# Kernel optimization log

Measured on AMD Instinct MI355X. Metric: run time of the kernel, lower is better.

Reference implementation:

```python
import jax, jax.numpy as jnp
import numpy as np

HID = 64   # RNN_HID_SIZE
FEAT = 9   # feature dim, hard-coded in module
T = 36     # SEQ_LEN


def setup_inputs() -> dict:
    key = jax.random.key(0)
    ks = jax.random.split(key, 20)
    B = 16384

    def u(k, shape, stdv):
        return jax.random.uniform(k, shape, jnp.float32, -stdv, stdv)

    s_h = 1.0 / np.sqrt(HID)    # stdv for layers with 64 rows / fan-in 64
    s_f = 1.0 / np.sqrt(FEAT)   # stdv 1/3 for feature-sized layers
    s_c = 1.0 / np.sqrt(2 * FEAT)  # weight_combine: Linear(18, 9)

    inp = {
        "values": jax.random.normal(ks[0], (B, T, FEAT), jnp.float32),
        "masks": (jax.random.uniform(ks[1], (B, T, FEAT)) < 0.8).astype(jnp.float32),
        "deltas": jax.random.uniform(ks[2], (B, T, FEAT), jnp.float32, 0.0, 5.0),
        # TemporalDecay h: W [64, 9], stdv = 1/sqrt(64)
        "W_gh": u(ks[3], (HID, FEAT), s_h), "b_gh": u(ks[4], (HID,), s_h),
        # TemporalDecay x (diag): W [9, 9], stdv = 1/sqrt(9)
        "W_gx": u(ks[5], (FEAT, FEAT), s_f), "b_gx": u(ks[6], (FEAT,), s_f),
        # hist_reg: Linear(64, 9)
        "W_hist": u(ks[7], (FEAT, HID), s_h), "b_hist": u(ks[8], (FEAT,), s_h),
        "W_feat": u(ks[9], (FEAT, FEAT), s_f), "b_feat": u(ks[10], (FEAT,), s_f),
        # weight_combine: Linear(18, 9)
        "W_comb": u(ks[11], (FEAT, 2 * FEAT), s_c), "b_comb": u(ks[12], (FEAT,), s_c),
        # LSTMCell(18, 64): gates order i, f, g, o
        "W_ih": u(ks[13], (4 * HID, 2 * FEAT), s_h), "W_hh": u(ks[14], (4 * HID, HID), s_h),
        "b_ih": u(ks[15], (4 * HID,), s_h), "b_hh": u(ks[16], (4 * HID,), s_h),
    }
    return inp


def reference(values, masks, deltas, W_gh, b_gh, W_gx, b_gx, W_hist, b_hist,
              W_feat, b_feat, W_comb, b_comb, W_ih, W_hh, b_ih, b_hh):
    B = values.shape[0]
    dt = values.dtype
    eye = jnp.eye(FEAT, dtype=dt)
    Wgx_diag = W_gx * eye            # TemporalDecay diag mask
    Wfeat_off = W_feat * (1.0 - eye)

    # time-major for scan: [T, B, F]
    xs = (jnp.swapaxes(values, 0, 1), jnp.swapaxes(masks, 0, 1), jnp.swapaxes(deltas, 0, 1))

    def step(carry, xt):
        h, c, loss = carry
        x, m, d = xt
        gamma_h = jnp.exp(-jax.nn.relu(d @ W_gh.T + b_gh))   # [B, 64]
        gamma_x = jnp.exp(-jax.nn.relu(d @ Wgx_diag.T + b_gx))  # [B, 9]
        h = h * gamma_h
        x_h = h @ W_hist.T + b_hist
        denom = jnp.sum(m) + 1e-5
        x_c = m * x + (1.0 - m) * x_h
        z_h = x_c @ Wfeat_off.T + b_feat
        alpha = jnp.concatenate([gamma_x, m], axis=1) @ W_comb.T + b_comb
        c_h = alpha * z_h + (1.0 - alpha) * x_h
        loss = loss + (jnp.sum(jnp.abs(x - x_h) * m)
                       + jnp.sum(jnp.abs(x - z_h) * m)
                       + jnp.sum(jnp.abs(x - c_h) * m)) / denom
        c_c = m * x + (1.0 - m) * c_h
        inp = jnp.concatenate([c_c, m], axis=1)              # [B, 18]
        gates = inp @ W_ih.T + b_ih + h @ W_hh.T + b_hh      # [B, 256]
        i, f, g, o = jnp.split(gates, 4, axis=1)
        c = jax.nn.sigmoid(f) * c + jax.nn.sigmoid(i) * jnp.tanh(g)
        h = jax.nn.sigmoid(o) * jnp.tanh(c)
        return (h, c, loss), c_c

    init = (jnp.zeros((B, HID), dt), jnp.zeros((B, HID), dt), jnp.zeros((), dt))
    (_, _, loss), imps = jax.lax.scan(step, init, xs)
    imputations = jnp.swapaxes(imps, 0, 1)  # [B, T, F]
    return loss / T, imputations
```

## Files before the change

### kernel.cpp

```cpp
#include <hip/hip_runtime.h>

typedef _Float16 hh;
typedef _Float16 h2  __attribute__((ext_vector_type(2)));
typedef _Float16 v4h __attribute__((ext_vector_type(4)));
typedef _Float16 v8h __attribute__((ext_vector_type(8)));
typedef float v4f    __attribute__((ext_vector_type(4)));
typedef unsigned short u16;

#define T_STEPS 36
#define FEAT 9
#define HID 64
#define BT 32
#define SIN_STR 232
#define PK_STR 40

__device__ __forceinline__ float fast_exp2(float x) {
#if __has_builtin(__builtin_amdgcn_exp2f)
  return __builtin_amdgcn_exp2f(x);
#else
  return exp2f(x);
#endif
}
__device__ __forceinline__ float fast_rcp(float x) {
#if __has_builtin(__builtin_amdgcn_rcpf)
  return __builtin_amdgcn_rcpf(x);
#else
  return 1.f / x;
#endif
}
__device__ __forceinline__ float sigmoid_fast(float x) {
  return fast_rcp(1.f + fast_exp2(x * -1.442695041f));
}
__device__ __forceinline__ float tanh_fast(float x) {
  return 1.f - 2.f * fast_rcp(1.f + fast_exp2(x * 2.885390082f));
}
__device__ __forceinline__ float fdot2(h2 a, h2 b, float c) {
#if __has_builtin(__builtin_amdgcn_fdot2)
  return __builtin_amdgcn_fdot2(a, b, c, false);
#else
  return c + (float)a[0] * (float)b[0] + (float)a[1] * (float)b[1];
#endif
}
__device__ __forceinline__ h2 mkh2(hh a, hh b) { h2 r; r[0] = a; r[1] = b; return r; }
__device__ __forceinline__ v4f mfma16(v8h a, v8h b, v4f c) {
  return __builtin_amdgcn_mfma_f32_16x16x32_f16(a, b, c, 0, 0, 0);
}

__global__ void zero_ws(float* __restrict__ ws, float* __restrict__ out) {
  int tid = threadIdx.x;
  if (tid < T_STEPS) ws[tid] = 0.f;
  if (tid == 0) out[0] = 0.f;
}

__global__ __launch_bounds__(256) void denom_kernel(const float* __restrict__ masks,
                                                    float* __restrict__ ws) {
  __shared__ float red[T_STEPS];
  const int tid = threadIdx.x;
  if (tid < T_STEPS) red[tid] = 0.f;
  __syncthreads();
  const int idx = blockIdx.x * 256 + tid;
  const int t0 = (idx % 9) * 4;
  const float4* p = (const float4*)masks + (size_t)idx * 9;
  float acc[4] = {0.f, 0.f, 0.f, 0.f};
#pragma unroll
  for (int c = 0; c < 9; ++c) {
    float4 v = p[c];
    acc[(4 * c) / 9]     += v.x;
    acc[(4 * c + 1) / 9] += v.y;
    acc[(4 * c + 2) / 9] += v.z;
    acc[(4 * c + 3) / 9] += v.w;
  }
#pragma unroll
  for (int j = 0; j < 4; ++j) atomicAdd(&red[t0 + j], acc[j]);
  __syncthreads();
  if (tid < T_STEPS) atomicAdd(&ws[tid], red[tid]);
}

#define BARX() asm volatile("s_waitcnt lgkmcnt(0)\n\ts_barrier" ::: "memory")

#define RITS_STEP(t, pxC,pmC,pdC,pxCb,pmCb,pdCb, pxN,pmN,pdN,pxNb,pmNb,pdNb)   \
  {                                                                            \
    const float inv_den = fast_rcp(denom[(t)] + 1e-5f);                        \
        \
    v4f gacc[2];                                                               \
    {                                                                          \
      const int sel = ((t) + 1) & 1;                                           \
      const int awin = 176 + sel * 24;                                         \
      _Pragma("unroll")                                                        \
      for (int mt = 0; mt < 2; ++mt) {                                         \
        v8h a_ = *(const v8h*)&sIn[(mt * 16 + nlo) * SIN_STR + awin + q * 8];  \
        v4f z4 = {0.f, 0.f, 0.f, 0.f};                                         \
        gacc[mt] = sel ? mfma16(a_, bGamB, z4) : mfma16(a_, bGamA, z4);        \
      }                                                                        \
    }                                                                          \
    if (wid < 2) {                                                             \
      const int base_ = ((t) & 1) * 96;                                        \
      v4f xacc = {0.f, 0.f, 0.f, 0.f};                                         \
      _Pragma("unroll")                                                        \
      for (int kt = 0; kt < 3; ++kt) {                                         \
        v8h a_ = *(const v8h*)&sIn[(wid * 16 + nlo) * SIN_STR + base_ +        \
                                   kt * 32 + q * 8];                           \
        xacc = mfma16(a_, bH[kt], xacc);                                       \
      }                                                                        \
      if (nlo < 9) {                                                           \
        _Pragma("unroll")                                                      \
        for (int r = 0; r < 4; ++r)                                            \
          sPk[(wid * 16 + q * 4 + r) * PK_STR + 18 + nlo] = (hh)xacc[r];       \
      }                                                                        \
    }                                                                          \
    BARX();                                                                    \
        \
    {                                                                          \
      const int pk = eP * PK_STR;                                              \
      float x_f  = (float)sPk[pk + fqw];                                       \
      float m_f  = (float)sPk[pk + 9 + fqw];                                   \
      float xh_f = (float)sPk[pk + 18 + fqw];                                  \
      v8h r0 = *(const v8h*)&sPk[pk];                                          \
      v8h r1 = *(const v8h*)&sPk[pk + 8];                                      \
      v8h r2 = *(const v8h*)&sPk[pk + 16];                                     \
      v8h r3 = *(const v8h*)&sPk[pk + 24];                                     \
      v4h r4 = *(const v4h*)&sPk[pk + 32];                                     \
      hh xxh[9] = {r0[0],r0[1],r0[2],r0[3],r0[4],r0[5],r0[6],r0[7],r1[0]};     \
      hh mmh[9] = {r1[1],r1[2],r1[3],r1[4],r1[5],r1[6],r1[7],r2[0],r2[1]};     \
      hh xhh[9] = {r2[2],r2[3],r2[4],r2[5],r2[6],r2[7],r3[0],r3[1],r3[2]};     \
      hh ddh[9] = {r3[3],r3[4],r3[5],r3[6],r3[7],r4[0],r4[1],r4[2],r4[3]};     \
      hh xch[10];                                                              \
      _Pragma("unroll")                                                        \
      for (int f = 0; f < 9; ++f) {                                            \
        u16 mb = __builtin_bit_cast(u16, mmh[f]);                              \
        xch[f] = mb ? xxh[f] : xhh[f];                                         \
      }                                                                        \
      xch[9] = (hh)0.f;                                                        \
      hh gxh[9];                                                               \
      _Pragma("unroll")                                                        \
      for (int f = 0; f < 9; ++f) {                                            \
        float y = fmaxf((float)ddh[f] * wgx[f] + bgxv[f], 0.f);                \
        gxh[f] = (hh)fast_exp2(y * -1.442695041f);                             \
      }                                                                        \
      h2 xc2[5] = {mkh2(xch[0],xch[1]), mkh2(xch[2],xch[3]),                   \
                   mkh2(xch[4],xch[5]), mkh2(xch[6],xch[7]),                   \
                   mkh2(xch[8],xch[9])};                                       \
      h2 g2[9]  = {mkh2(gxh[0],gxh[1]), mkh2(gxh[2],gxh[3]),                   \
                   mkh2(gxh[4],gxh[5]), mkh2(gxh[6],gxh[7]),                   \
                   mkh2(gxh[8],mmh[0]), mkh2(mmh[1],mmh[2]),                   \
                   mkh2(mmh[3],mmh[4]), mkh2(mmh[5],mmh[6]),                   \
                   mkh2(mmh[7],mmh[8])};                                       \
      float z1 = bf1, a1 = bc1v;                                               \
      _Pragma("unroll")                                                        \
      for (int j = 0; j < 5; ++j) z1 = fdot2(wf1[j], xc2[j], z1);              \
      _Pragma("unroll")                                                        \
      for (int j = 0; j < 9; ++j) a1 = fdot2(wc1[j], g2[j], a1);               \
      float ch1 = xh_f + a1 * (z1 - xh_f);                                     \
      bool obs1 = (m_f != 0.f);                                                \
      float cc1 = obs1 ? x_f : ch1;                                            \
      float lterm = obs1 ? (fabsf(x_f - xh_f) + fabsf(x_f - z1) +              \
                            fabsf(x_f - ch1)) : 0.f;                           \
      const int pb = ((t) & 1) * 96;                                           \
      sIn[eP * SIN_STR + pb + fqw] = (hh)cc1;                                  \
      sIn[eP * SIN_STR + pb + 9 + fqw] = (hh)m_f;                              \
      out[1 + (size_t)(b0 + eP) * (T_STEPS * FEAT) + (t) * FEAT + fqw] = cc1;  \
      if (fqw == 7) {                                                          \
        float z2 = bf2, a2 = bc2v;                                             \
        _Pragma("unroll")                                                      \
        for (int j = 0; j < 5; ++j) z2 = fdot2(wf2[j], xc2[j], z2);            \
        _Pragma("unroll")                                                      \
        for (int j = 0; j < 9; ++j) a2 = fdot2(wc2[j], g2[j], a2);             \
        float x8 = (float)xxh[8], m8 = (float)mmh[8], xh8 = (float)xhh[8];     \
        float ch2 = xh8 + a2 * (z2 - xh8);                                     \
        bool obs2 = (m8 != 0.f);                                               \
        float cc2 = obs2 ? x8 : ch2;                                           \
        lterm += obs2 ? (fabsf(x8 - xh8) + fabsf(x8 - z2) +                    \
                         fabsf(x8 - ch2)) : 0.f;                               \
        sIn[eP * SIN_STR + pb + 8] = (hh)cc2;                                  \
        sIn[eP * SIN_STR + pb + 17] = mmh[8];                                  \
        out[1 + (size_t)(b0 + eP) * (T_STEPS * FEAT) + (t) * FEAT + 8] = cc2;  \
      }                                                                        \
      loss_acc += lterm * inv_den;                                             \
    }                                                                          \
    BARX();                                                                    \
      \
    {                                                                          \
      const bool ldN = ((t) + 2 < T_STEPS);                                    \
      const bool ldD = ((t) + 3 < T_STEPS);                                    \
      if (ldN) {                                                               \
        size_t offn = (size_t)(b0 + e1) * (T_STEPS * FEAT) +                   \
                      ((t) + 2) * FEAT + f1;                                   \
        pxN = values[offn]; pmN = masks[offn];                                 \
        if (tid < 32) {                                                        \
          size_t offn2 = (size_t)(b0 + e2g) * (T_STEPS * FEAT) +               \
                         ((t) + 2) * FEAT + f2g;                               \
          pxNb = values[offn2]; pmNb = masks[offn2];                           \
        }                                                                      \
      }                                                                        \
      if (ldD) {                                                               \
        size_t offd = (size_t)(b0 + e1) * (T_STEPS * FEAT) +                   \
                      ((t) + 3) * FEAT + f1;                                   \
        pdN = deltas[offd];                                                    \
        if (tid < 32) {                                                        \
          size_t offd2 = (size_t)(b0 + e2g) * (T_STEPS * FEAT) +               \
                         ((t) + 3) * FEAT + f2g;                               \
          pdNb = deltas[offd2];                                                \
        }                                                                      \
      }                                                                        \
      const int base_ = ((t) & 1) * 96;                                        \
      const int pub = (((t) + 1) & 1) * 96;                                    \
      v8h af[2][3];                                                            \
      _Pragma("unroll")                                                        \
      for (int mt = 0; mt < 2; ++mt)                                           \
        _Pragma("unroll")                                                      \
        for (int kt = 0; kt < 3; ++kt)                                         \
          af[mt][kt] = *(const v8h*)&sIn[(mt * 16 + nlo) * SIN_STR + base_ +   \
                                         kt * 32 + q * 8];                     \
      v4f acc[2][4];                                                           \
      _Pragma("unroll")                                                        \
      for (int mt = 0; mt < 2; ++mt)                                           \
        _Pragma("unroll")                                                      \
        for (int p = 0; p < 4; ++p)                                            \
          acc[mt][p] = (v4f){0.f, 0.f, 0.f, 0.f};                              \
      _Pragma("unroll")                                                        \
      for (int mt = 0; mt < 2; ++mt)                                           \
        _Pragma("unroll")                                                      \
        for (int p = 0; p < 4; ++p)                                            \
          _Pragma("unroll")                                                    \
          for (int kt = 0; kt < 3; ++kt)                                       \
            acc[mt][p] = mfma16(af[mt][kt], bG[p][kt], acc[mt][p]);            \
      _Pragma("unroll")                                                        \
      for (int mt = 0; mt < 2; ++mt) {                                         \
        _Pragma("unroll")                                                      \
        for (int r = 0; r < 4; ++r) {                                          \
          float ig = sigmoid_fast(acc[mt][0][r]);                              \
          float fg = sigmoid_fast(acc[mt][1][r]);                              \
          float gg = tanh_fast(acc[mt][2][r]);                                 \
          float og = sigmoid_fast(acc[mt][3][r]);                              \
          float cn = fg * c_s[mt * 4 + r] + ig * gg;                           \
          c_s[mt * 4 + r] = cn;                                                \
          float hn = og * tanh_fast(cn);                                       \
          float gam = fast_exp2(fmaxf(gacc[mt][r], 0.f) * -1.442695041f);      \
          sIn[(mt * 16 + q * 4 + r) * SIN_STR + pub + 18 + j_col] =            \
              (hh)(hn * gam);                                                  \
        }                                                                      \
      }                                                                        \
      if ((t) + 1 < T_STEPS) {                                                 \
        sPk[e1 * PK_STR + f1] = (hh)pxC;                                       \
        sPk[e1 * PK_STR + 9 + f1] = (hh)pmC;                                   \
        sPk[e1 * PK_STR + 27 + f1] = (hh)dH;                                   \
        if (tid < 32) {                                                        \
          sPk[e2g * PK_STR + f2g] = (hh)pxCb;                                  \
          sPk[e2g * PK_STR + 9 + f2g] = (hh)pmCb;                              \
          sPk[e2g * PK_STR + 27 + f2g] = (hh)dHb;                              \
        }                                                                      \
      }                                                                        \
      if ((t) + 2 < T_STEPS) {                                                 \
        const int sb = 192 + ((t) & 1) * 10;                                   \
        sIn[e1 * SIN_STR + sb + f1] = (hh)pdC;                                 \
        if (tid < 32) sIn[e2g * SIN_STR + sb + f2g] = (hh)pdCb;                \
      }                                                                        \
      dH = pdC; dHb = pdCb;                                                    \
    }                                                                          \
    BARX();                                                                    \
  }

__global__ __launch_bounds__(256, 2) void rits_kernel(
    const float* __restrict__ values, const float* __restrict__ masks,
    const float* __restrict__ deltas,
    const float* __restrict__ W_gh, const float* __restrict__ b_gh,
    const float* __restrict__ W_gx, const float* __restrict__ b_gx,
    const float* __restrict__ W_hist, const float* __restrict__ b_hist,
    const float* __restrict__ W_feat, const float* __restrict__ b_feat,
    const float* __restrict__ W_comb, const float* __restrict__ b_comb,
    const float* __restrict__ W_ih, const float* __restrict__ W_hh,
    const float* __restrict__ b_ih, const float* __restrict__ b_hh,
    const float* __restrict__ denom, float* __restrict__ out) {

  __shared__ __align__(16) hh sIn[BT * SIN_STR];
  __shared__ __align__(16) hh sPk[BT * PK_STR];
  __shared__ float sRed[256];

  const int tid = threadIdx.x;
  const int lane = tid & 63;
  const int wid = tid >> 6;
  const int q = lane >> 4;
  const int nlo = lane & 15;
  const int b0 = blockIdx.x * BT;
  const int j_col = 16 * wid + nlo;

  v8h bG[4][3];
#pragma unroll
  for (int p = 0; p < 4; ++p)
#pragma unroll
    for (int kt = 0; kt < 3; ++kt) {
      int n = 64 * p + j_col;
      v8h r;
#pragma unroll
      for (int jj = 0; jj < 8; ++jj) {
        int k = kt * 32 + q * 8 + jj;
        float v = 0.f;
        if (k < 18)       v = W_ih[n * 18 + k];
        else if (k < 82)  v = W_hh[n * 64 + (k - 18)];
        else if (k == 82) v = b_ih[n] + b_hh[n];
        r[jj] = (hh)v;
      }
      bG[p][kt] = r;
    }
  v8h bH[3];
#pragma unroll
  for (int kt = 0; kt < 3; ++kt) {
    v8h r;
#pragma unroll
    for (int jj = 0; jj < 8; ++jj) {
      int k = kt * 32 + q * 8 + jj;
      float v = 0.f;
      if (nlo < 9) {
        if (k >= 18 && k < 82) v = W_hist[nlo * 64 + (k - 18)];
        else if (k == 82)      v = b_hist[nlo];
      }
      r[jj] = (hh)v;
    }
    bH[kt] = r;
  }
  v8h bGamA, bGamB;
  {
    int n = j_col;
    v8h ra, rb;
#pragma unroll
    for (int jj = 0; jj < 8; ++jj) {
      int k = q * 8 + jj;
      float va = 0.f, vb = 0.f;
      if (k == 2) va = b_gh[n];
      else if (k >= 16 && k < 25) va = W_gh[n * 9 + (k - 16)];
      if (k >= 2 && k < 11) vb = W_gh[n * 9 + (k - 2)];
      else if (k == 12) vb = b_gh[n];
      ra[jj] = (hh)va; rb[jj] = (hh)vb;
    }
    bGamA = ra; bGamB = rb;
  }

  const int eP = tid >> 3, fqw = tid & 7;
  h2 wf1[5], wf2[5], wc1[9], wc2[9];
  float bf1 = b_feat[fqw], bf2 = b_feat[8];
  float bc1v = b_comb[fqw], bc2v = b_comb[8];
#pragma unroll
  for (int j = 0; j < 5; ++j) {
    int i0 = 2 * j, i1 = 2 * j + 1;
    hh a0 = (hh)((i0 == fqw) ? 0.f : W_feat[fqw * 9 + i0]);
    hh a1 = (hh)((i1 < 9) ? ((i1 == fqw) ? 0.f : W_feat[fqw * 9 + i1]) : 0.f);
    wf1[j] = mkh2(a0, a1);
    hh c0 = (hh)((i0 == 8) ? 0.f : W_feat[8 * 9 + i0]);
    hh c1 = (hh)((i1 < 9) ? W_feat[8 * 9 + i1] : 0.f);
    wf2[j] = mkh2(c0, c1);
  }
#pragma unroll
  for (int j = 0; j < 9; ++j) {
    wc1[j] = mkh2((hh)W_comb[fqw * 18 + 2 * j], (hh)W_comb[fqw * 18 + 2 * j + 1]);
    wc2[j] = mkh2((hh)W_comb[8 * 18 + 2 * j], (hh)W_comb[8 * 18 + 2 * j + 1]);
  }
  float wgx[9], bgxv[9];
#pragma unroll
  for (int f = 0; f < 9; ++f) { wgx[f] = W_gx[f * 9 + f]; bgxv[f] = b_gx[f]; }

  for (int i = tid; i < BT * SIN_STR; i += 256) sIn[i] = (hh)0.f;
  __syncthreads();
  if (tid < BT) {
    sIn[tid * SIN_STR + 82] = (hh)1.f;
    sIn[tid * SIN_STR + 178] = (hh)1.f;
    sIn[tid * SIN_STR + 212] = (hh)1.f;
  }
  const int e1 = tid / 9, f1 = tid - 9 * e1;
  const int e2g = (tid + 256) / 9, f2g = (tid + 256) - 9 * e2g;
  float pA_x = 0.f, pA_m = 0.f, pA_d = 0.f, pA_xb = 0.f, pA_mb = 0.f, pA_db = 0.f;
  float pB_x = 0.f, pB_m = 0.f, pB_d = 0.f, pB_xb = 0.f, pB_mb = 0.f, pB_db = 0.f;
  float dH = 0.f, dHb = 0.f;
  {
    size_t off = (size_t)(b0 + e1) * (T_STEPS * FEAT) + f1;
    sPk[e1 * PK_STR + f1] = (hh)values[off];
    sPk[e1 * PK_STR + 9 + f1] = (hh)masks[off];
    sPk[e1 * PK_STR + 27 + f1] = (hh)deltas[off];
    float d1 = deltas[off + FEAT];
    dH = d1;
    sIn[e1 * SIN_STR + 202 + f1] = (hh)d1;
    pA_x = values[off + FEAT]; pA_m = masks[off + FEAT];
    pA_d = deltas[off + 2 * FEAT];
    if (tid < 32) {
      size_t off2 = (size_t)(b0 + e2g) * (T_STEPS * FEAT) + f2g;
      sPk[e2g * PK_STR + f2g] = (hh)values[off2];
      sPk[e2g * PK_STR + 9 + f2g] = (hh)masks[off2];
      sPk[e2g * PK_STR + 27 + f2g] = (hh)deltas[off2];
      float d1b = deltas[off2 + FEAT];
      dHb = d1b;
      sIn[e2g * SIN_STR + 202 + f2g] = (hh)d1b;
      pA_xb = values[off2 + FEAT]; pA_mb = masks[off2 + FEAT];
      pA_db = deltas[off2 + 2 * FEAT];
    }
  }
  __syncthreads();

  float c_s[8];
#pragma unroll
  for (int i = 0; i < 8; ++i) c_s[i] = 0.f;
  float loss_acc = 0.f;

  for (int t = 0; t < T_STEPS; t += 2) {
    RITS_STEP(t,     pA_x, pA_m, pA_d, pA_xb, pA_mb, pA_db,
                     pB_x, pB_m, pB_d, pB_xb, pB_mb, pB_db);
    RITS_STEP(t + 1, pB_x, pB_m, pB_d, pB_xb, pB_mb, pB_db,
                     pA_x, pA_m, pA_d, pA_xb, pA_mb, pA_db);
  }

  sRed[tid] = loss_acc;
  __syncthreads();
  for (int k = 128; k > 0; k >>= 1) {
    if (tid < k) sRed[tid] += sRed[tid + k];
    __syncthreads();
  }
  if (tid == 0) atomicAdd(out, sRed[0] * (1.f / (float)T_STEPS));
}

extern "C" void kernel_launch(void* const* d_in, const int* in_sizes, int n_in,
                              void* d_out, int out_size, void* d_ws, size_t ws_size,
                              hipStream_t stream) {
  const float* values = (const float*)d_in[0];
  const float* masks  = (const float*)d_in[1];
  const float* deltas = (const float*)d_in[2];
  const float* W_gh   = (const float*)d_in[3];
  const float* b_gh   = (const float*)d_in[4];
  const float* W_gx   = (const float*)d_in[5];
  const float* b_gx   = (const float*)d_in[6];
  const float* W_hist = (const float*)d_in[7];
  const float* b_hist = (const float*)d_in[8];
  const float* W_feat = (const float*)d_in[9];
  const float* b_feat = (const float*)d_in[10];
  const float* W_comb = (const float*)d_in[11];
  const float* b_comb = (const float*)d_in[12];
  const float* W_ih   = (const float*)d_in[13];
  const float* W_hh   = (const float*)d_in[14];
  const float* b_ih   = (const float*)d_in[15];
  const float* b_hh   = (const float*)d_in[16];

  float* out = (float*)d_out;
  float* ws  = (float*)d_ws;
  int B = in_sizes[0] / (T_STEPS * FEAT);

  zero_ws<<<1, 64, 0, stream>>>(ws, out);
  denom_kernel<<<(B * 9) / 256, 256, 0, stream>>>(masks, ws);
  rits_kernel<<<B / BT, 256, 0, stream>>>(values, masks, deltas,
                                          W_gh, b_gh, W_gx, b_gx,
                                          W_hist, b_hist, W_feat, b_feat,
                                          W_comb, b_comb, W_ih, W_hh,
                                          b_ih, b_hh, ws, out);
}
```

Measured before the change: 242.9 us.

## Drop per-step barrier by redundant x_h MFMA per wave; precompute gamma_x at staging

Every wave now computes the history-regression MFMA for its own row tile, so each wave has the x_h values it needs without the block barrier. That barrier is replaced by a local LDS wait. Gamma_x is now computed once per element when deltas are staged into shared memory, instead of redundantly (9 exps) per thread per step. The fdot2 chains are split into independent accumulators to shorten dependency latency. The trade-off is extra redundant MFMA work, and skipping the barrier may risk cross-wave data races on the shared buffers.

```diff
diff --git a/kernel.cpp b/kernel.cpp
--- a/kernel.cpp
+++ b/kernel.cpp
@@ -81,7 +81,8 @@
 #define RITS_STEP(t, pxC,pmC,pdC,pxCb,pmCb,pdCb, pxN,pmN,pdN,pxNb,pmNb,pdNb)   \
   {                                                                            \
     const float inv_den = fast_rcp(denom[(t)] + 1e-5f);                        \
-        \
+    const int pb = ((t) & 1) * 96;                                             \
+         \
     v4f gacc[2];                                                               \
     {                                                                          \
       const int sel = ((t) + 1) & 1;                                           \
@@ -93,23 +94,25 @@
         gacc[mt] = sel ? mfma16(a_, bGamB, z4) : mfma16(a_, bGamA, z4);        \
       }                                                                        \
     }                                                                          \
-    if (wid < 2) {                                                             \
-      const int base_ = ((t) & 1) * 96;                                        \
+       \
+    {                                                                          \
       v4f xacc = {0.f, 0.f, 0.f, 0.f};                                         \
       _Pragma("unroll")                                                        \
       for (int kt = 0; kt < 3; ++kt) {                                         \
-        v8h a_ = *(const v8h*)&sIn[(wid * 16 + nlo) * SIN_STR + base_ +        \
+        v8h a_ = *(const v8h*)&sIn[(mtw * 16 + nlo) * SIN_STR + pb +           \
                                    kt * 32 + q * 8];                           \
         xacc = mfma16(a_, bH[kt], xacc);                                       \
       }                                                                        \
-      if (nlo < 9) {                                                           \
+         \
+      if ((q >> 1) == (wid & 1) && nlo < 9) {                                  \
         _Pragma("unroll")                                                      \
         for (int r = 0; r < 4; ++r)                                            \
-          sPk[(wid * 16 + q * 4 + r) * PK_STR + 18 + nlo] = (hh)xacc[r];       \
+          sPk[(mtw * 16 + q * 4 + r) * PK_STR + 18 + nlo] = (hh)xacc[r];       \
       }                                                                        \
     }                                                                          \
-    BARX();                                                                    \
-        \
+           \
+    asm volatile("s_waitcnt lgkmcnt(0)" ::: "memory");                         \
+                 \
     {                                                                          \
       const int pk = eP * PK_STR;                                              \
       float x_f  = (float)sPk[pk + fqw];                                       \
@@ -123,7 +126,7 @@
       hh xxh[9] = {r0[0],r0[1],r0[2],r0[3],r0[4],r0[5],r0[6],r0[7],r1[0]};     \
       hh mmh[9] = {r1[1],r1[2],r1[3],r1[4],r1[5],r1[6],r1[7],r2[0],r2[1]};     \
       hh xhh[9] = {r2[2],r2[3],r2[4],r2[5],r2[6],r2[7],r3[0],r3[1],r3[2]};     \
-      hh ddh[9] = {r3[3],r3[4],r3[5],r3[6],r3[7],r4[0],r4[1],r4[2],r4[3]};     \
+      hh gxh[9] = {r3[3],r3[4],r3[5],r3[6],r3[7],r4[0],r4[1],r4[2],r4[3]};     \
       hh xch[10];                                                              \
       _Pragma("unroll")                                                        \
       for (int f = 0; f < 9; ++f) {                                            \
@@ -131,12 +134,6 @@
         xch[f] = mb ? xxh[f] : xhh[f];                                         \
       }                                                                        \
       xch[9] = (hh)0.f;                                                        \
-      hh gxh[9];                                                               \
-      _Pragma("unroll")                                                        \
-      for (int f = 0; f < 9; ++f) {                                            \
-        float y = fmaxf((float)ddh[f] * wgx[f] + bgxv[f], 0.f);                \
-        gxh[f] = (hh)fast_exp2(y * -1.442695041f);                             \
-      }                                                                        \
       h2 xc2[5] = {mkh2(xch[0],xch[1]), mkh2(xch[2],xch[3]),                   \
                    mkh2(xch[4],xch[5]), mkh2(xch[6],xch[7]),                   \
                    mkh2(xch[8],xch[9])};                                       \
@@ -145,26 +142,40 @@
                    mkh2(gxh[8],mmh[0]), mkh2(mmh[1],mmh[2]),                   \
                    mkh2(mmh[3],mmh[4]), mkh2(mmh[5],mmh[6]),                   \
                    mkh2(mmh[7],mmh[8])};                                       \
-      float z1 = bf1, a1 = bc1v;                                               \
-      _Pragma("unroll")                                                        \
-      for (int j = 0; j < 5; ++j) z1 = fdot2(wf1[j], xc2[j], z1);              \
-      _Pragma("unroll")                                                        \
-      for (int j = 0; j < 9; ++j) a1 = fdot2(wc1[j], g2[j], a1);               \
+                        \
+      float z1a = bf1, z1b = 0.f;                                              \
+      z1a = fdot2(wf1[0], xc2[0], z1a); z1b = fdot2(wf1[1], xc2[1], z1b);      \
+      z1a = fdot2(wf1[2], xc2[2], z1a); z1b = fdot2(wf1[3], xc2[3], z1b);      \
+      z1a = fdot2(wf1[4], xc2[4], z1a);                                        \
+      float z1 = z1a + z1b;                                                    \
+      float a1a = bc1v, a1b = 0.f, a1c = 0.f;                                  \
+      a1a = fdot2(wc1[0], g2[0], a1a); a1b = fdot2(wc1[1], g2[1], a1b);        \
+      a1c = fdot2(wc1[2], g2[2], a1c); a1a = fdot2(wc1[3], g2[3], a1a);        \
+      a1b = fdot2(wc1[4], g2[4], a1b); a1c = fdot2(wc1[5], g2[5], a1c);        \
+      a1a = fdot2(wc1[6], g2[6], a1a); a1b = fdot2(wc1[7], g2[7], a1b);        \
+      a1c = fdot2(wc1[8], g2[8], a1c);                                         \
+      float a1 = (a1a + a1b) + a1c;                                            \
       float ch1 = xh_f + a1 * (z1 - xh_f);                                     \
       bool obs1 = (m_f != 0.f);                                                \
       float cc1 = obs1 ? x_f : ch1;                                            \
       float lterm = obs1 ? (fabsf(x_f - xh_f) + fabsf(x_f - z1) +              \
                             fabsf(x_f - ch1)) : 0.f;                           \
-      const int pb = ((t) & 1) * 96;                                           \
       sIn[eP * SIN_STR + pb + fqw] = (hh)cc1;                                  \
       sIn[eP * SIN_STR + pb + 9 + fqw] = (hh)m_f;                              \
       out[1 + (size_t)(b0 + eP) * (T_STEPS * FEAT) + (t) * FEAT + fqw] = cc1;  \
       if (fqw == 7) {                                                          \
-        float z2 = bf2, a2 = bc2v;                                             \
-        _Pragma("unroll")                                                      \
-        for (int j = 0; j < 5; ++j) z2 = fdot2(wf2[j], xc2[j], z2);            \
-        _Pragma("unroll")                                                      \
-        for (int j = 0; j < 9; ++j) a2 = fdot2(wc2[j], g2[j], a2);             \
+        float z2a = bf2, z2b = 0.f;                                            \
+        z2a = fdot2(wf2[0], xc2[0], z2a); z2b = fdot2(wf2[1], xc2[1], z2b);    \
+        z2a = fdot2(wf2[2], xc2[2], z2a); z2b = fdot2(wf2[3], xc2[3], z2b);    \
+        z2a = fdot2(wf2[4], xc2[4], z2a);                                      \
+        float z2 = z2a + z2b;                                                  \
+        float a2a = bc2v, a2b = 0.f, a2c = 0.f;                                \
+        a2a = fdot2(wc2[0], g2[0], a2a); a2b = fdot2(wc2[1], g2[1], a2b);      \
+        a2c = fdot2(wc2[2], g2[2], a2c); a2a = fdot2(wc2[3], g2[3], a2a);      \
+        a2b = fdot2(wc2[4], g2[4], a2b); a2c = fdot2(wc2[5], g2[5], a2c);      \
+        a2a = fdot2(wc2[6], g2[6], a2a); a2b = fdot2(wc2[7], g2[7], a2b);      \
+        a2c = fdot2(wc2[8], g2[8], a2c);                                       \
+        float a2 = (a2a + a2b) + a2c;                                          \
         float x8 = (float)xxh[8], m8 = (float)mmh[8], xh8 = (float)xhh[8];     \
         float ch2 = xh8 + a2 * (z2 - xh8);                                     \
         bool obs2 = (m8 != 0.f);                                               \
@@ -202,14 +213,13 @@
           pdNb = deltas[offd2];                                                \
         }                                                                      \
       }                                                                        \
-      const int base_ = ((t) & 1) * 96;                                        \
       const int pub = (((t) + 1) & 1) * 96;                                    \
       v8h af[2][3];                                                            \
       _Pragma("unroll")                                                        \
       for (int mt = 0; mt < 2; ++mt)                                           \
         _Pragma("unroll")                                                      \
         for (int kt = 0; kt < 3; ++kt)                                         \
-          af[mt][kt] = *(const v8h*)&sIn[(mt * 16 + nlo) * SIN_STR + base_ +   \
+          af[mt][kt] = *(const v8h*)&sIn[(mt * 16 + nlo) * SIN_STR + pb +      \
                                          kt * 32 + q * 8];                     \
       v4f acc[2][4];                                                           \
       _Pragma("unroll")                                                        \
@@ -243,11 +253,13 @@
       if ((t) + 1 < T_STEPS) {                                                 \
         sPk[e1 * PK_STR + f1] = (hh)pxC;                                       \
         sPk[e1 * PK_STR + 9 + f1] = (hh)pmC;                                   \
-        sPk[e1 * PK_STR + 27 + f1] = (hh)dH;                                   \
+        sPk[e1 * PK_STR + 27 + f1] =                                           \
+            (hh)fast_exp2(fmaxf(dH * wgx1 + bgx1, 0.f) * -1.442695041f);       \
         if (tid < 32) {                                                        \
           sPk[e2g * PK_STR + f2g] = (hh)pxCb;                                  \
           sPk[e2g * PK_STR + 9 + f2g] = (hh)pmCb;                              \
-          sPk[e2g * PK_STR + 27 + f2g] = (hh)dHb;                              \
+          sPk[e2g * PK_STR + 27 + f2g] =                                       \
+              (hh)fast_exp2(fmaxf(dHb * wgx2 + bgx2, 0.f) * -1.442695041f);    \
         }                                                                      \
       }                                                                        \
       if ((t) + 2 < T_STEPS) {                                                 \
@@ -283,6 +295,7 @@
   const int nlo = lane & 15;
   const int b0 = blockIdx.x * BT;
   const int j_col = 16 * wid + nlo;
+  const int mtw = wid >> 1;
 
   v8h bG[4][3];
 #pragma unroll
@@ -354,9 +367,12 @@
     wc1[j] = mkh2((hh)W_comb[fqw * 18 + 2 * j], (hh)W_comb[fqw * 18 + 2 * j + 1]);
     wc2[j] = mkh2((hh)W_comb[8 * 18 + 2 * j], (hh)W_comb[8 * 18 + 2 * j + 1]);
   }
-  float wgx[9], bgxv[9];
-#pragma unroll
-  for (int f = 0; f < 9; ++f) { wgx[f] = W_gx[f * 9 + f]; bgxv[f] = b_gx[f]; }
+
+  const int e1 = tid / 9, f1 = tid - 9 * e1;
+  const int e2g = (tid + 256) / 9, f2g = (tid + 256) - 9 * e2g;
+  const float wgx1 = W_gx[f1 * 9 + f1], bgx1 = b_gx[f1];
+  float wgx2 = 0.f, bgx2 = 0.f;
+  if (tid < 32) { wgx2 = W_gx[f2g * 9 + f2g]; bgx2 = b_gx[f2g]; }
 
   for (int i = tid; i < BT * SIN_STR; i += 256) sIn[i] = (hh)0.f;
   __syncthreads();
@@ -365,16 +381,16 @@
     sIn[tid * SIN_STR + 178] = (hh)1.f;
     sIn[tid * SIN_STR + 212] = (hh)1.f;
   }
-  const int e1 = tid / 9, f1 = tid - 9 * e1;
-  const int e2g = (tid + 256) / 9, f2g = (tid + 256) - 9 * e2g;
   float pA_x = 0.f, pA_m = 0.f, pA_d = 0.f, pA_xb = 0.f, pA_mb = 0.f, pA_db = 0.f;
   float pB_x = 0.f, pB_m = 0.f, pB_d = 0.f, pB_xb = 0.f, pB_mb = 0.f, pB_db = 0.f;
   float dH = 0.f, dHb = 0.f;
   {
     size_t off = (size_t)(b0 + e1) * (T_STEPS * FEAT) + f1;
+    float d0 = deltas[off];
     sPk[e1 * PK_STR + f1] = (hh)values[off];
     sPk[e1 * PK_STR + 9 + f1] = (hh)masks[off];
-    sPk[e1 * PK_STR + 27 + f1] = (hh)deltas[off];
+    sPk[e1 * PK_STR + 27 + f1] =
+        (hh)fast_exp2(fmaxf(d0 * wgx1 + bgx1, 0.f) * -1.442695041f);
     float d1 = deltas[off + FEAT];
     dH = d1;
     sIn[e1 * SIN_STR + 202 + f1] = (hh)d1;
@@ -382,9 +398,11 @@
     pA_d = deltas[off + 2 * FEAT];
     if (tid < 32) {
       size_t off2 = (size_t)(b0 + e2g) * (T_STEPS * FEAT) + f2g;
+      float d0b = deltas[off2];
       sPk[e2g * PK_STR + f2g] = (hh)values[off2];
       sPk[e2g * PK_STR + 9 + f2g] = (hh)masks[off2];
-      sPk[e2g * PK_STR + 27 + f2g] = (hh)deltas[off2];
+      sPk[e2g * PK_STR + 27 + f2g] =
+          (hh)fast_exp2(fmaxf(d0b * wgx2 + bgx2, 0.f) * -1.442695041f);
       float d1b = deltas[off2 + FEAT];
       dHb = d1b;
       sIn[e2g * SIN_STR + 202 + f2g] = (hh)d1b;
```

New measurement: 245.4 us. Within noise of the previous version (+1.0%).

## Give each wavefront its own 16-row batch tile to drop block barriers

Applied to the files above, without the earlier changes.

The block work split changes from 4 waves sharing 32 batch rows (each wave owning a slice of hidden columns) to each wave owning an independent 16-row tile and computing all 256 gate columns. Workgroup s_barriers become wave-local LDS waitcnt fences, and the feature stage is split so each lane handles 3 features of one element. The gamma_x exponential is also precomputed when deltas are staged. In exchange, each wave holds 48 gate weight fragments and 16 cell-state values in registers, so launch bounds drop to one block per SIMD pair and occupancy falls.

```diff
diff --git a/kernel.cpp b/kernel.cpp
--- a/kernel.cpp
+++ b/kernel.cpp
@@ -10,7 +10,8 @@
 #define T_STEPS 36
 #define FEAT 9
 #define HID 64
-#define BT 32
+#define WT 16
+#define NW 4
 #define SIN_STR 232
 #define PK_STR 40
 
@@ -76,45 +77,44 @@
   if (tid < T_STEPS) atomicAdd(&ws[tid], red[tid]);
 }
 
-#define BARX() asm volatile("s_waitcnt lgkmcnt(0)\n\ts_barrier" ::: "memory")
-
-#define RITS_STEP(t, pxC,pmC,pdC,pxCb,pmCb,pdCb, pxN,pmN,pdN,pxNb,pmNb,pdNb)   \
+#define WFENCE() do { \
+  asm volatile("s_waitcnt lgkmcnt(0)" ::: "memory"); \
+  __builtin_amdgcn_sched_barrier(0); \
+} while (0)
+
+#define STEP(t, CUR, NXT)                                                      \
   {                                                                            \
     const float inv_den = fast_rcp(denom[(t)] + 1e-5f);                        \
-        \
-    v4f gacc[2];                                                               \
+    const int pb = ((t) & 1) * 96;                                             \
+    const int pub = (((t) + 1) & 1) * 96;                                      \
+               \
+    v4f gacc[4];                                                               \
     {                                                                          \
       const int sel = ((t) + 1) & 1;                                           \
       const int awin = 176 + sel * 24;                                         \
-      _Pragma("unroll")                                                        \
-      for (int mt = 0; mt < 2; ++mt) {                                         \
-        v8h a_ = *(const v8h*)&sIn[(mt * 16 + nlo) * SIN_STR + awin + q * 8];  \
-        v4f z4 = {0.f, 0.f, 0.f, 0.f};                                         \
-        gacc[mt] = sel ? mfma16(a_, bGamB, z4) : mfma16(a_, bGamA, z4);        \
-      }                                                                        \
+      v8h ag = *(const v8h*)&sIn[nlo * SIN_STR + awin + q * 8];                \
+      v4f z4 = {0.f, 0.f, 0.f, 0.f};                                           \
+      _Pragma("unroll")                                                        \
+      for (int p = 0; p < 4; ++p)                                              \
+        gacc[p] = sel ? mfma16(ag, bGamB[p], z4) : mfma16(ag, bGamA[p], z4);   \
     }                                                                          \
-    if (wid < 2) {                                                             \
-      const int base_ = ((t) & 1) * 96;                                        \
+    {                                                                          \
       v4f xacc = {0.f, 0.f, 0.f, 0.f};                                         \
       _Pragma("unroll")                                                        \
       for (int kt = 0; kt < 3; ++kt) {                                         \
-        v8h a_ = *(const v8h*)&sIn[(wid * 16 + nlo) * SIN_STR + base_ +        \
-                                   kt * 32 + q * 8];                           \
+        v8h a_ = *(const v8h*)&sIn[nlo * SIN_STR + pb + kt * 32 + q * 8];      \
         xacc = mfma16(a_, bH[kt], xacc);                                       \
       }                                                                        \
       if (nlo < 9) {                                                           \
         _Pragma("unroll")                                                      \
         for (int r = 0; r < 4; ++r)                                            \
-          sPk[(wid * 16 + q * 4 + r) * PK_STR + 18 + nlo] = (hh)xacc[r];       \
+          sPk[(q * 4 + r) * PK_STR + 18 + nlo] = (hh)xacc[r];                  \
       }                                                                        \
     }                                                                          \
-    BARX();                                                                    \
-        \
-    {                                                                          \
-      const int pk = eP * PK_STR;                                              \
-      float x_f  = (float)sPk[pk + fqw];                                       \
-      float m_f  = (float)sPk[pk + 9 + fqw];                                   \
-      float xh_f = (float)sPk[pk + 18 + fqw];                                  \
+    WFENCE();                                                                  \
+                   \
+    if (s < 3) {                                                               \
+      const int pk = e * PK_STR;                                               \
       v8h r0 = *(const v8h*)&sPk[pk];                                          \
       v8h r1 = *(const v8h*)&sPk[pk + 8];                                      \
       v8h r2 = *(const v8h*)&sPk[pk + 16];                                     \
@@ -123,7 +123,7 @@
       hh xxh[9] = {r0[0],r0[1],r0[2],r0[3],r0[4],r0[5],r0[6],r0[7],r1[0]};     \
       hh mmh[9] = {r1[1],r1[2],r1[3],r1[4],r1[5],r1[6],r1[7],r2[0],r2[1]};     \
       hh xhh[9] = {r2[2],r2[3],r2[4],r2[5],r2[6],r2[7],r3[0],r3[1],r3[2]};     \
-      hh ddh[9] = {r3[3],r3[4],r3[5],r3[6],r3[7],r4[0],r4[1],r4[2],r4[3]};     \
+      hh gxh[9] = {r3[3],r3[4],r3[5],r3[6],r3[7],r4[0],r4[1],r4[2],r4[3]};     \
       hh xch[10];                                                              \
       _Pragma("unroll")                                                        \
       for (int f = 0; f < 9; ++f) {                                            \
@@ -131,12 +131,6 @@
         xch[f] = mb ? xxh[f] : xhh[f];                                         \
       }                                                                        \
       xch[9] = (hh)0.f;                                                        \
-      hh gxh[9];                                                               \
-      _Pragma("unroll")                                                        \
-      for (int f = 0; f < 9; ++f) {                                            \
-        float y = fmaxf((float)ddh[f] * wgx[f] + bgxv[f], 0.f);                \
-        gxh[f] = (hh)fast_exp2(y * -1.442695041f);                             \
-      }                                                                        \
       h2 xc2[5] = {mkh2(xch[0],xch[1]), mkh2(xch[2],xch[3]),                   \
                    mkh2(xch[4],xch[5]), mkh2(xch[6],xch[7]),                   \
                    mkh2(xch[8],xch[9])};                                       \
@@ -145,122 +139,106 @@
                    mkh2(gxh[8],mmh[0]), mkh2(mmh[1],mmh[2]),                   \
                    mkh2(mmh[3],mmh[4]), mkh2(mmh[5],mmh[6]),                   \
                    mkh2(mmh[7],mmh[8])};                                       \
-      float z1 = bf1, a1 = bc1v;                                               \
-      _Pragma("unroll")                                                        \
-      for (int j = 0; j < 5; ++j) z1 = fdot2(wf1[j], xc2[j], z1);              \
-      _Pragma("unroll")                                                        \
-      for (int j = 0; j < 9; ++j) a1 = fdot2(wc1[j], g2[j], a1);               \
-      float ch1 = xh_f + a1 * (z1 - xh_f);                                     \
-      bool obs1 = (m_f != 0.f);                                                \
-      float cc1 = obs1 ? x_f : ch1;                                            \
-      float lterm = obs1 ? (fabsf(x_f - xh_f) + fabsf(x_f - z1) +              \
-                            fabsf(x_f - ch1)) : 0.f;                           \
-      const int pb = ((t) & 1) * 96;                                           \
-      sIn[eP * SIN_STR + pb + fqw] = (hh)cc1;                                  \
-      sIn[eP * SIN_STR + pb + 9 + fqw] = (hh)m_f;                              \
-      out[1 + (size_t)(b0 + eP) * (T_STEPS * FEAT) + (t) * FEAT + fqw] = cc1;  \
-      if (fqw == 7) {                                                          \
-        float z2 = bf2, a2 = bc2v;                                             \
-        _Pragma("unroll")                                                      \
-        for (int j = 0; j < 5; ++j) z2 = fdot2(wf2[j], xc2[j], z2);            \
-        _Pragma("unroll")                                                      \
-        for (int j = 0; j < 9; ++j) a2 = fdot2(wc2[j], g2[j], a2);             \
-        float x8 = (float)xxh[8], m8 = (float)mmh[8], xh8 = (float)xhh[8];     \
-        float ch2 = xh8 + a2 * (z2 - xh8);                                     \
-        bool obs2 = (m8 != 0.f);                                               \
-        float cc2 = obs2 ? x8 : ch2;                                           \
-        lterm += obs2 ? (fabsf(x8 - xh8) + fabsf(x8 - z2) +                    \
-                         fabsf(x8 - ch2)) : 0.f;                               \
-        sIn[eP * SIN_STR + pb + 8] = (hh)cc2;                                  \
-        sIn[eP * SIN_STR + pb + 17] = mmh[8];                                  \
-        out[1 + (size_t)(b0 + eP) * (T_STEPS * FEAT) + (t) * FEAT + 8] = cc2;  \
+      float lterm = 0.f;                                                       \
+      _Pragma("unroll")                                                        \
+      for (int j = 0; j < 3; ++j) {                                            \
+        const int f = 3 * s + j;                                               \
+        float x_f  = (float)sPk[pk + f];                                       \
+        float m_f  = (float)sPk[pk + 9 + f];                                   \
+        float xh_f = (float)sPk[pk + 18 + f];                                  \
+        float za = bf[j], zb = 0.f;                                            \
+        za = fdot2(wf[j][0], xc2[0], za); zb = fdot2(wf[j][1], xc2[1], zb);    \
+        za = fdot2(wf[j][2], xc2[2], za); zb = fdot2(wf[j][3], xc2[3], zb);    \
+        za = fdot2(wf[j][4], xc2[4], za);                                      \
+        float z = za + zb;                                                     \
+        float aa = bc[j], ab = 0.f, ac = 0.f;                                  \
+        aa = fdot2(wc[j][0], g2[0], aa); ab = fdot2(wc[j][1], g2[1], ab);      \
+        ac = fdot2(wc[j][2], g2[2], ac); aa = fdot2(wc[j][3], g2[3], aa);      \
+        ab = fdot2(wc[j][4], g2[4], ab); ac = fdot2(wc[j][5], g2[5], ac);      \
+        aa = fdot2(wc[j][6], g2[6], aa); ab = fdot2(wc[j][7], g2[7], ab);      \
+        ac = fdot2(wc[j][8], g2[8], ac);                                       \
+        float a = (aa + ab) + ac;                                              \
+        float ch = xh_f + a * (z - xh_f);                                      \
+        bool obs = (m_f != 0.f);                                               \
+        float cc = obs ? x_f : ch;                                             \
+        lterm += obs ? (fabsf(x_f - xh_f) + fabsf(x_f - z) +                   \
+                        fabsf(x_f - ch)) : 0.f;                                \
+        sIn[e * SIN_STR + pb + f] = (hh)cc;                                    \
+        sIn[e * SIN_STR + pb + 9 + f] = (hh)m_f;                               \
+        outp[j] = cc;                                                          \
       }                                                                        \
       loss_acc += lterm * inv_den;                                             \
     }                                                                          \
-    BARX();                                                                    \
+    WFENCE();                                                                  \
       \
     {                                                                          \
-      const bool ldN = ((t) + 2 < T_STEPS);                                    \
-      const bool ldD = ((t) + 3 < T_STEPS);                                    \
-      if (ldN) {                                                               \
-        size_t offn = (size_t)(b0 + e1) * (T_STEPS * FEAT) +                   \
-                      ((t) + 2) * FEAT + f1;                                   \
-        pxN = values[offn]; pmN = masks[offn];                                 \
-        if (tid < 32) {                                                        \
-          size_t offn2 = (size_t)(b0 + e2g) * (T_STEPS * FEAT) +               \
-                         ((t) + 2) * FEAT + f2g;                               \
-          pxNb = values[offn2]; pmNb = masks[offn2];                           \
+      if (s < 3) {                                                             \
+        if ((t) + 2 < T_STEPS) {                                               \
+          _Pragma("unroll")                                                    \
+          for (int j = 0; j < 3; ++j) {                                        \
+            p##NXT##_x[j] = vp[18 + j];                                        \
+            p##NXT##_m[j] = mp[18 + j];                                        \
+          }                                                                    \
         }                                                                      \
-      }                                                                        \
-      if (ldD) {                                                               \
-        size_t offd = (size_t)(b0 + e1) * (T_STEPS * FEAT) +                   \
-                      ((t) + 3) * FEAT + f1;                                   \
-        pdN = deltas[offd];                                                    \
-        if (tid < 32) {                                                        \
-          size_t offd2 = (size_t)(b0 + e2g) * (T_STEPS * FEAT) +               \
-                         ((t) + 3) * FEAT + f2g;                               \
-          pdNb = deltas[offd2];                                                \
+        if ((t) + 3 < T_STEPS) {                                               \
+          _Pragma("unroll")                                                    \
+          for (int j = 0; j < 3; ++j) p##NXT##_d[j] = dp[27 + j];              \
         }                                                                      \
       }                                                                        \
-      const int base_ = ((t) & 1) * 96;                                        \
-      const int pub = (((t) + 1) & 1) * 96;                                    \
-      v8h af[2][3];                                                            \
-      _Pragma("unroll")                                                        \
-      for (int mt = 0; mt < 2; ++mt)                                           \
+      v8h af[3];                                                               \
+      _Pragma("unroll")                                                        \
+      for (int kt = 0; kt < 3; ++kt)                                           \
+        af[kt] = *(const v8h*)&sIn[nlo * SIN_STR + pb + kt * 32 + q * 8];      \
+      v4f acc[16];                                                             \
+      _Pragma("unroll")                                                        \
+      for (int p = 0; p < 16; ++p) acc[p] = (v4f){0.f, 0.f, 0.f, 0.f};         \
+      _Pragma("unroll")                                                        \
+      for (int p = 0; p < 16; ++p)                                             \
         _Pragma("unroll")                                                      \
         for (int kt = 0; kt < 3; ++kt)                                         \
-          af[mt][kt] = *(const v8h*)&sIn[(mt * 16 + nlo) * SIN_STR + base_ +   \
-                                         kt * 32 + q * 8];                     \
-      v4f acc[2][4];                                                           \
-      _Pragma("unroll")                                                        \
-      for (int mt = 0; mt < 2; ++mt)                                           \
-        _Pragma("unroll")                                                      \
-        for (int p = 0; p < 4; ++p)                                            \
-          acc[mt][p] = (v4f){0.f, 0.f, 0.f, 0.f};                              \
-      _Pragma("unroll")                                                        \
-      for (int mt = 0; mt < 2; ++mt)                                           \
-        _Pragma("unroll")                                                      \
-        for (int p = 0; p < 4; ++p)                                            \
-          _Pragma("unroll")                                                    \
-          for (int kt = 0; kt < 3; ++kt)                                       \
-            acc[mt][p] = mfma16(af[mt][kt], bG[p][kt], acc[mt][p]);            \
-      _Pragma("unroll")                                                        \
-      for (int mt = 0; mt < 2; ++mt) {                                         \
+          acc[p] = mfma16(af[kt], bG[p][kt], acc[p]);                          \
+      _Pragma("unroll")                                                        \
+      for (int p = 0; p < 4; ++p) {                                            \
         _Pragma("unroll")                                                      \
         for (int r = 0; r < 4; ++r) {                                          \
-          float ig = sigmoid_fast(acc[mt][0][r]);                              \
-          float fg = sigmoid_fast(acc[mt][1][r]);                              \
-          float gg = tanh_fast(acc[mt][2][r]);                                 \
-          float og = sigmoid_fast(acc[mt][3][r]);                              \
-          float cn = fg * c_s[mt * 4 + r] + ig * gg;                           \
-          c_s[mt * 4 + r] = cn;                                                \
+          float ig = sigmoid_fast(acc[p][r]);                                  \
+          float fg = sigmoid_fast(acc[p + 4][r]);                              \
+          float gg = tanh_fast(acc[p + 8][r]);                                 \
+          float og = sigmoid_fast(acc[p + 12][r]);                             \
+          float cn = fg * c_s[p * 4 + r] + ig * gg;                            \
+          c_s[p * 4 + r] = cn;                                                 \
           float hn = og * tanh_fast(cn);                                       \
-          float gam = fast_exp2(fmaxf(gacc[mt][r], 0.f) * -1.442695041f);      \
-          sIn[(mt * 16 + q * 4 + r) * SIN_STR + pub + 18 + j_col] =            \
+          float gam = fast_exp2(fmaxf(gacc[p][r], 0.f) * -1.442695041f);       \
+          sIn[(q * 4 + r) * SIN_STR + pub + 18 + 16 * p + nlo] =               \
               (hh)(hn * gam);                                                  \
         }                                                                      \
       }                                                                        \
-      if ((t) + 1 < T_STEPS) {                                                 \
-        sPk[e1 * PK_STR + f1] = (hh)pxC;                                       \
-        sPk[e1 * PK_STR + 9 + f1] = (hh)pmC;                                   \
-        sPk[e1 * PK_STR + 27 + f1] = (hh)dH;                                   \
-        if (tid < 32) {                                                        \
-          sPk[e2g * PK_STR + f2g] = (hh)pxCb;                                  \
-          sPk[e2g * PK_STR + 9 + f2g] = (hh)pmCb;                              \
-          sPk[e2g * PK_STR + 27 + f2g] = (hh)dHb;                              \
+      if (s < 3) {                                                             \
+        if ((t) + 1 < T_STEPS) {                                               \
+          _Pragma("unroll")                                                    \
+          for (int j = 0; j < 3; ++j) {                                        \
+            sPk[e * PK_STR + 3 * s + j] = (hh)p##CUR##_x[j];                   \
+            sPk[e * PK_STR + 9 + 3 * s + j] = (hh)p##CUR##_m[j];               \
+            sPk[e * PK_STR + 27 + 3 * s + j] =                                 \
+                (hh)fast_exp2(fmaxf(dH[j] * wgx[j] + bgx[j], 0.f) *            \
+                              -1.442695041f);                                  \
+          }                                                                    \
         }                                                                      \
-      }                                                                        \
-      if ((t) + 2 < T_STEPS) {                                                 \
-        const int sb = 192 + ((t) & 1) * 10;                                   \
-        sIn[e1 * SIN_STR + sb + f1] = (hh)pdC;                                 \
-        if (tid < 32) sIn[e2g * SIN_STR + sb + f2g] = (hh)pdCb;                \
-      }                                                                        \
-      dH = pdC; dHb = pdCb;                                                    \
+        if ((t) + 2 < T_STEPS) {                                               \
+          const int sb = 192 + ((t) & 1) * 10;                                 \
+          _Pragma("unroll")                                                    \
+          for (int j = 0; j < 3; ++j) {                                        \
+            sIn[e * SIN_STR + sb + 3 * s + j] = (hh)p##CUR##_d[j];             \
+            dH[j] = p##CUR##_d[j];                                             \
+          }                                                                    \
+        }                                                                      \
+      }                                                                        \
+      vp += FEAT; mp += FEAT; dp += FEAT; outp += FEAT;                        \
     }                                                                          \
-    BARX();                                                                    \
-  }
-
-__global__ __launch_bounds__(256, 2) void rits_kernel(
+    WFENCE();                                                                  \
+  }
+
+__global__ __launch_bounds__(256, 1) void rits_kernel(
     const float* __restrict__ values, const float* __restrict__ masks,
     const float* __restrict__ deltas,
     const float* __restrict__ W_gh, const float* __restrict__ b_gh,
@@ -272,24 +250,27 @@
     const float* __restrict__ b_ih, const float* __restrict__ b_hh,
     const float* __restrict__ denom, float* __restrict__ out) {
 
-  __shared__ __align__(16) hh sIn[BT * SIN_STR];
-  __shared__ __align__(16) hh sPk[BT * PK_STR];
+  __shared__ __align__(16) hh sInAll[NW * WT * SIN_STR];
+  __shared__ __align__(16) hh sPkAll[NW * WT * PK_STR];
   __shared__ float sRed[256];
 
   const int tid = threadIdx.x;
   const int lane = tid & 63;
-  const int wid = tid >> 6;
+  const int w = tid >> 6;
   const int q = lane >> 4;
   const int nlo = lane & 15;
-  const int b0 = blockIdx.x * BT;
-  const int j_col = 16 * wid + nlo;
-
-  v8h bG[4][3];
-#pragma unroll
-  for (int p = 0; p < 4; ++p)
+  const int e = lane >> 2;
+  const int s = lane & 3;
+  hh* sIn = sInAll + w * WT * SIN_STR;
+  hh* sPk = sPkAll + w * WT * PK_STR;
+  const int b0w = blockIdx.x * (NW * WT) + w * WT;
+
+  v8h bG[16][3];
+#pragma unroll
+  for (int p = 0; p < 16; ++p)
 #pragma unroll
     for (int kt = 0; kt < 3; ++kt) {
-      int n = 64 * p + j_col;
+      int n = 16 * p + nlo;
       v8h r;
 #pragma unroll
       for (int jj = 0; jj < 8; ++jj) {
@@ -318,9 +299,10 @@
     }
     bH[kt] = r;
   }
-  v8h bGamA, bGamB;
-  {
-    int n = j_col;
+  v8h bGamA[4], bGamB[4];
+#pragma unroll
+  for (int p = 0; p < 4; ++p) {
+    int n = 16 * p + nlo;
     v8h ra, rb;
 #pragma unroll
     for (int jj = 0; jj < 8; ++jj) {
@@ -332,78 +314,72 @@
       else if (k == 12) vb = b_gh[n];
       ra[jj] = (hh)va; rb[jj] = (hh)vb;
     }
-    bGamA = ra; bGamB = rb;
-  }
-
-  const int eP = tid >> 3, fqw = tid & 7;
-  h2 wf1[5], wf2[5], wc1[9], wc2[9];
-  float bf1 = b_feat[fqw], bf2 = b_feat[8];
-  float bc1v = b_comb[fqw], bc2v = b_comb[8];
-#pragma unroll
-  for (int j = 0; j < 5; ++j) {
-    int i0 = 2 * j, i1 = 2 * j + 1;
-    hh a0 = (hh)((i0 == fqw) ? 0.f : W_feat[fqw * 9 + i0]);
-    hh a1 = (hh)((i1 < 9) ? ((i1 == fqw) ? 0.f : W_feat[fqw * 9 + i1]) : 0.f);
-    wf1[j] = mkh2(a0, a1);
-    hh c0 = (hh)((i0 == 8) ? 0.f : W_feat[8 * 9 + i0]);
-    hh c1 = (hh)((i1 < 9) ? W_feat[8 * 9 + i1] : 0.f);
-    wf2[j] = mkh2(c0, c1);
-  }
-#pragma unroll
-  for (int j = 0; j < 9; ++j) {
-    wc1[j] = mkh2((hh)W_comb[fqw * 18 + 2 * j], (hh)W_comb[fqw * 18 + 2 * j + 1]);
-    wc2[j] = mkh2((hh)W_comb[8 * 18 + 2 * j], (hh)W_comb[8 * 18 + 2 * j + 1]);
-  }
-  float wgx[9], bgxv[9];
-#pragma unroll
-  for (int f = 0; f < 9; ++f) { wgx[f] = W_gx[f * 9 + f]; bgxv[f] = b_gx[f]; }
-
-  for (int i = tid; i < BT * SIN_STR; i += 256) sIn[i] = (hh)0.f;
-  __syncthreads();
-  if (tid < BT) {
-    sIn[tid * SIN_STR + 82] = (hh)1.f;
-    sIn[tid * SIN_STR + 178] = (hh)1.f;
-    sIn[tid * SIN_STR + 212] = (hh)1.f;
-  }
-  const int e1 = tid / 9, f1 = tid - 9 * e1;
-  const int e2g = (tid + 256) / 9, f2g = (tid + 256) - 9 * e2g;
-  float pA_x = 0.f, pA_m = 0.f, pA_d = 0.f, pA_xb = 0.f, pA_mb = 0.f, pA_db = 0.f;
-  float pB_x = 0.f, pB_m = 0.f, pB_d = 0.f, pB_xb = 0.f, pB_mb = 0.f, pB_db = 0.f;
-  float dH = 0.f, dHb = 0.f;
-  {
-    size_t off = (size_t)(b0 + e1) * (T_STEPS * FEAT) + f1;
-    sPk[e1 * PK_STR + f1] = (hh)values[off];
-    sPk[e1 * PK_STR + 9 + f1] = (hh)masks[off];
-    sPk[e1 * PK_STR + 27 + f1] = (hh)deltas[off];
-    float d1 = deltas[off + FEAT];
-    dH = d1;
-    sIn[e1 * SIN_STR + 202 + f1] = (hh)d1;
-    pA_x = values[off + FEAT]; pA_m = masks[off + FEAT];
-    pA_d = deltas[off + 2 * FEAT];
-    if (tid < 32) {
-      size_t off2 = (size_t)(b0 + e2g) * (T_STEPS * FEAT) + f2g;
-      sPk[e2g * PK_STR + f2g] = (hh)values[off2];
-      sPk[e2g * PK_STR + 9 + f2g] = (hh)masks[off2];
-      sPk[e2g * PK_STR + 27 + f2g] = (hh)deltas[off2];
-      float d1b = deltas[off2 + FEAT];
-      dHb = d1b;
-      sIn[e2g * SIN_STR + 202 + f2g] = (hh)d1b;
-      pA_xb = values[off2 + FEAT]; pA_mb = masks[off2 + FEAT];
-      pA_db = deltas[off2 + 2 * FEAT];
+    bGamA[p] = ra; bGamB[p] = rb;
+  }
+
+  const int sc = (s < 3) ? s : 0;
+  h2 wf[3][5], wc[3][9];
+  float bf[3], bc[3], wgx[3], bgx[3];
+#pragma unroll
+  for (int j = 0; j < 3; ++j) {
+    const int f = 3 * sc + j;
+    bf[j] = b_feat[f];
+    bc[j] = b_comb[f];
+    wgx[j] = W_gx[f * 9 + f];
+    bgx[j] = b_gx[f];
+#pragma unroll
+    for (int i = 0; i < 5; ++i) {
+      int i0 = 2 * i, i1 = 2 * i + 1;
+      hh a0 = (hh)((i0 == f) ? 0.f : W_feat[f * 9 + i0]);
+      hh a1 = (hh)((i1 < 9) ? ((i1 == f) ? 0.f : W_feat[f * 9 + i1]) : 0.f);
+      wf[j][i] = mkh2(a0, a1);
     }
-  }
-  __syncthreads();
-
-  float c_s[8];
-#pragma unroll
-  for (int i = 0; i < 8; ++i) c_s[i] = 0.f;
+#pragma unroll
+    for (int i = 0; i < 9; ++i)
+      wc[j][i] = mkh2((hh)W_comb[f * 18 + 2 * i], (hh)W_comb[f * 18 + 2 * i + 1]);
+  }
+
+  const size_t ebase = (size_t)(b0w + e) * (T_STEPS * FEAT) + 3 * sc;
+  const float* vp = values + ebase;
+  const float* mp = masks + ebase;
+  const float* dp = deltas + ebase;
+  float* outp = out + 1 + ebase;
+
+  for (int i = lane; i < WT * SIN_STR; i += 64) sIn[i] = (hh)0.f;
+  if (lane < WT) {
+    sIn[lane * SIN_STR + 82] = (hh)1.f;
+    sIn[lane * SIN_STR + 178] = (hh)1.f;
+    sIn[lane * SIN_STR + 212] = (hh)1.f;
+  }
+
+  float pA_x[3] = {0.f,0.f,0.f}, pA_m[3] = {0.f,0.f,0.f}, pA_d[3] = {0.f,0.f,0.f};
+  float pB_x[3] = {0.f,0.f,0.f}, pB_m[3] = {0.f,0.f,0.f}, pB_d[3] = {0.f,0.f,0.f};
+  float dH[3] = {0.f, 0.f, 0.f};
+  if (s < 3) {
+#pragma unroll
+    for (int j = 0; j < 3; ++j) {
+      float x0 = vp[j], m0 = mp[j], d0 = dp[j];
+      sPk[e * PK_STR + 3 * s + j] = (hh)x0;
+      sPk[e * PK_STR + 9 + 3 * s + j] = (hh)m0;
+      sPk[e * PK_STR + 27 + 3 * s + j] =
+          (hh)fast_exp2(fmaxf(d0 * wgx[j] + bgx[j], 0.f) * -1.442695041f);
+      float d1 = dp[FEAT + j];
+      dH[j] = d1;
+      sIn[e * SIN_STR + 202 + 3 * s + j] = (hh)d1;
+      pA_x[j] = vp[FEAT + j]; pA_m[j] = mp[FEAT + j];
+      pA_d[j] = dp[2 * FEAT + j];
+    }
+  }
+  WFENCE();
+
+  float c_s[16];
+#pragma unroll
+  for (int i = 0; i < 16; ++i) c_s[i] = 0.f;
   float loss_acc = 0.f;
 
   for (int t = 0; t < T_STEPS; t += 2) {
-    RITS_STEP(t,     pA_x, pA_m, pA_d, pA_xb, pA_mb, pA_db,
-                     pB_x, pB_m, pB_d, pB_xb, pB_mb, pB_db);
-    RITS_STEP(t + 1, pB_x, pB_m, pB_d, pB_xb, pB_mb, pB_db,
-                     pA_x, pA_m, pA_d, pA_xb, pA_mb, pA_db);
+    STEP(t,     A, B)
+    STEP(t + 1, B, A)
   }
 
   sRed[tid] = loss_acc;
@@ -442,9 +418,9 @@
 
   zero_ws<<<1, 64, 0, stream>>>(ws, out);
   denom_kernel<<<(B * 9) / 256, 256, 0, stream>>>(masks, ws);
-  rits_kernel<<<B / BT, 256, 0, stream>>>(values, masks, deltas,
-                                          W_gh, b_gh, W_gx, b_gx,
-                                          W_hist, b_hist, W_feat, b_feat,
-                                          W_comb, b_comb, W_ih, W_hh,
-                                          b_ih, b_hh, ws, out);
-}
+  rits_kernel<<<B / (NW * WT), 256, 0, stream>>>(values, masks, deltas,
+                                                 W_gh, b_gh, W_gx, b_gx,
+                                                 W_hist, b_hist, W_feat, b_feat,
+                                                 W_comb, b_comb, W_ih, W_hh,
+                                                 b_ih, b_hh, ws, out);
+}
```

Measured after the change: 337.9 us. +39.1%, slower.
